# Optimization experiments

Hardware: AMD Instinct MI355X
Metric: run time of the kernel (lower is better)

## Reference

```python
import jax, jax.numpy as jnp
import numpy as np
import math

N, IN, OUT, E, K = 50000, 256, 256, 800000, 32

def setup_inputs() -> dict:
    key = jax.random.key(0)
    k0, k1, k2, k3, k4 = jax.random.split(key, 5)
    feat = jax.random.normal(k0, (N, IN), dtype=jnp.float32)
    # xavier_uniform with relu gain, as in reset_parameters
    gain = math.sqrt(2.0)
    a = gain * math.sqrt(6.0 / (IN + OUT))
    W_self = jax.random.uniform(k1, (OUT, IN), minval=-a, maxval=a, dtype=jnp.float32)
    W_neigh = jax.random.uniform(k2, (OUT, IN), minval=-a, maxval=a, dtype=jnp.float32)
    b_neigh = jnp.zeros((OUT,), dtype=jnp.float32)
    # random CSR graph: E edges, row pointers from sorted cut points
    indices = jax.random.randint(k3, (E,), 0, N, dtype=jnp.int32)
    inner = jnp.sort(jax.random.randint(k4, (N - 1,), 0, E, dtype=jnp.int32))
    indptr = jnp.concatenate([jnp.zeros((1,), jnp.int32), inner,
                              jnp.full((1,), E, jnp.int32)])
    return {"feat": feat, "W_self": W_self, "W_neigh": W_neigh,
            "b_neigh": b_neigh, "indices": indices, "indptr": indptr}

def reference(feat, W_self, W_neigh, b_neigh, indices, indptr):
    n = feat.shape[0]
    # feat_drop with p=0.0 is identity
    h_self = feat @ W_self.T                      # [N, OUT]
    feat_neigh = feat @ W_neigh.T + b_neigh       # [N, OUT]
    # MaxK: keep top-k entries per row, zero the rest
    vals, idx = jax.lax.top_k(feat_neigh, K)      # [N, K]
    rows = jnp.arange(n)[:, None]
    masked = jnp.zeros_like(feat_neigh).at[rows, idx].set(vals)
    # CSR SpMM with unit values (sum over neighbors)
    deg = indptr[1:] - indptr[:-1]                # [N]
    dst = jnp.repeat(jnp.arange(n, dtype=jnp.int32), deg,
                     total_repeat_length=indices.shape[0])
    h_neigh = jax.ops.segment_sum(masked[indices], dst, num_segments=n)
    return h_self + h_neigh
```

## Files before the change

### kernel.cpp

```cpp
#include <hip/hip_runtime.h>

#define N_NODES 50000
#define TOPK 32
#define SOFT_DELTA 2e-5f

typedef unsigned long long u64;
typedef unsigned u32;
typedef float f32x16 __attribute__((ext_vector_type(16)));
typedef __bf16 bf16x8 __attribute__((ext_vector_type(8)));

__device__ __forceinline__ float dec(u32 u) {
    return __builtin_bit_cast(float, (u & 0x80000000u) ? (u & 0x7FFFFFFFu) : ~u);
}
__device__ __forceinline__ int mbcnt64(u64 m) {
    return __builtin_amdgcn_mbcnt_hi((u32)(m >> 32),
           __builtin_amdgcn_mbcnt_lo((u32)m, 0u));
}

__device__ __forceinline__ u32 enc4(float v, int col) {
    return ((u32)col << 16) |
           ((__builtin_bit_cast(u32, v) + 0x8000u) >> 16);
}

__device__ __forceinline__ u32 s2(float x0, float x1, float& r0, float& r1) {
    const u32 h0 = (__builtin_bit_cast(u32, x0) + 0x8000u) & 0xFFFF0000u;
    const u32 h1 = (__builtin_bit_cast(u32, x1) + 0x8000u) & 0xFFFF0000u;
    r0 = x0 - __builtin_bit_cast(float, h0);
    r1 = x1 - __builtin_bit_cast(float, h1);
    return (h0 >> 16) | h1;
}
__device__ __forceinline__ u32 p2(float x0, float x1) {
    return (((__builtin_bit_cast(u32, x0) + 0x8000u) & 0xFFFF0000u) >> 16) |
           ((__builtin_bit_cast(u32, x1) + 0x8000u) & 0xFFFF0000u);
}

struct Tri { uint4 h1, h2, h3; };
__device__ __forceinline__ Tri cvt8(const float4 u, const float4 v, bool deep) {
    Tri t;
    float r0,r1,r2,r3,r4,r5,r6,r7;
    t.h1.x = s2(u.x, u.y, r0, r1);
    t.h1.y = s2(u.z, u.w, r2, r3);
    t.h1.z = s2(v.x, v.y, r4, r5);
    t.h1.w = s2(v.z, v.w, r6, r7);
    float s0,s1,s2_,s3,s4,s5,s6,s7;
    t.h2.x = s2(r0, r1, s0, s1);
    t.h2.y = s2(r2, r3, s2_, s3);
    t.h2.z = s2(r4, r5, s4, s5);
    t.h2.w = s2(r6, r7, s6, s7);
    if (deep) {
        t.h3.x = p2(s0, s1); t.h3.y = p2(s2_, s3);
        t.h3.z = p2(s4, s5); t.h3.w = p2(s6, s7);
    } else {
        t.h3 = make_uint4(0, 0, 0, 0);
    }
    return t;
}

__global__ __launch_bounds__(256, 2) void gemm_kernel(
    const float* __restrict__ feat,
    const float* __restrict__ Wself,
    const float* __restrict__ Wneigh,
    const float* __restrict__ bneigh,
    float* __restrict__ hself,
    float* __restrict__ fneigh)
{
    __shared__ uint4 LA1[512], LA2[512], LA3[512];
    __shared__ uint4 LB1[512], LB2[512], LB3[512];

    const int tid  = threadIdx.x;
    const int lane = tid & 63;
    const int wave = tid >> 6;
    const int wm   = wave >> 1;
    const int wn   = wave & 1;
    const int kg   = lane >> 5;

    const int rowTile = blockIdx.x >> 2;
    const int colTile = blockIdx.x & 3;
    const int row0 = rowTile * 128;
    const float* __restrict__ Wbase = (colTile < 2) ? Wself : Wneigh;
    const int jbase = (colTile & 1) << 7;
    const bool deep = (colTile >= 2);

    const int srow  = tid >> 1;
    const int shalf = tid & 1;
    int gra = row0 + srow;
    if (gra >= N_NODES) gra = 0;
    const float* pa = feat  + (size_t)gra * 256 + shalf * 16;
    const float* pb = Wbase + (size_t)(jbase + srow) * 256 + shalf * 16;
    const int i0 = ((shalf * 2) << 7) + srow;
    const int i1 = i0 + 128;

    const int rA0 = wm * 64 + (lane & 31);
    const int rB0 = wn * 64 + (lane & 31);

    f32x16 acc[2][2];
#pragma unroll
    for (int i = 0; i < 2; ++i)
#pragma unroll
        for (int j = 0; j < 2; ++j) acc[i][j] = (f32x16)0.f;

    float4 va0, va1, va2, va3, vb0, vb1, vb2, vb3;
    va0 = *(const float4*)(pa);      va1 = *(const float4*)(pa + 4);
    va2 = *(const float4*)(pa + 8);  va3 = *(const float4*)(pa + 12);
    vb0 = *(const float4*)(pb);      vb1 = *(const float4*)(pb + 4);
    vb2 = *(const float4*)(pb + 8);  vb3 = *(const float4*)(pb + 12);

    for (int s = 0; s < 8; ++s) {
        __syncthreads();
        {
            const Tri tA0 = cvt8(va0, va1, deep);
            const Tri tA1 = cvt8(va2, va3, deep);
            const Tri tB0 = cvt8(vb0, vb1, deep);
            const Tri tB1 = cvt8(vb2, vb3, deep);
            LA1[i0] = tA0.h1; LA2[i0] = tA0.h2;
            LA1[i1] = tA1.h1; LA2[i1] = tA1.h2;
            LB1[i0] = tB0.h1; LB2[i0] = tB0.h2;
            LB1[i1] = tB1.h1; LB2[i1] = tB1.h2;
            if (deep) {
                LA3[i0] = tA0.h3; LA3[i1] = tA1.h3;
                LB3[i0] = tB0.h3; LB3[i1] = tB1.h3;
            }
        }
        __syncthreads();

        if (s < 7) {
            const int ko = (s + 1) * 32;
            va0 = *(const float4*)(pa + ko);      va1 = *(const float4*)(pa + ko + 4);
            va2 = *(const float4*)(pa + ko + 8);  va3 = *(const float4*)(pa + ko + 12);
            vb0 = *(const float4*)(pb + ko);      vb1 = *(const float4*)(pb + ko + 4);
            vb2 = *(const float4*)(pb + ko + 8);  vb3 = *(const float4*)(pb + ko + 12);
        }

        if (deep) {
#pragma unroll
            for (int ks = 0; ks < 2; ++ks) {
                const int base = ((ks << 1) | kg) << 7;
                bf16x8 a1[2], a2[2], a3[2], b1[2], b2[2], b3[2];
#pragma unroll
                for (int f = 0; f < 2; ++f) {
                    const int ia = base + rA0 + f * 32;
                    const int ib = base + rB0 + f * 32;
                    a1[f] = __builtin_bit_cast(bf16x8, LA1[ia]);
                    a2[f] = __builtin_bit_cast(bf16x8, LA2[ia]);
                    a3[f] = __builtin_bit_cast(bf16x8, LA3[ia]);
                    b1[f] = __builtin_bit_cast(bf16x8, LB1[ib]);
                    b2[f] = __builtin_bit_cast(bf16x8, LB2[ib]);
                    b3[f] = __builtin_bit_cast(bf16x8, LB3[ib]);
                }
#pragma unroll
                for (int i = 0; i < 2; ++i)
#pragma unroll
                    for (int j = 0; j < 2; ++j) {
                        acc[i][j] = __builtin_amdgcn_mfma_f32_32x32x16_bf16(
                            a1[i], b1[j], acc[i][j], 0, 0, 0);
                        acc[i][j] = __builtin_amdgcn_mfma_f32_32x32x16_bf16(
                            a1[i], b2[j], acc[i][j], 0, 0, 0);
                        acc[i][j] = __builtin_amdgcn_mfma_f32_32x32x16_bf16(
                            a2[i], b1[j], acc[i][j], 0, 0, 0);
                        acc[i][j] = __builtin_amdgcn_mfma_f32_32x32x16_bf16(
                            a2[i], b2[j], acc[i][j], 0, 0, 0);
                        acc[i][j] = __builtin_amdgcn_mfma_f32_32x32x16_bf16(
                            a1[i], b3[j], acc[i][j], 0, 0, 0);
                        acc[i][j] = __builtin_amdgcn_mfma_f32_32x32x16_bf16(
                            a3[i], b1[j], acc[i][j], 0, 0, 0);
                    }
            }
        } else {
#pragma unroll
            for (int ks = 0; ks < 2; ++ks) {
                const int base = ((ks << 1) | kg) << 7;
                bf16x8 a1[2], a2[2], b1[2], b2[2];
#pragma unroll
                for (int f = 0; f < 2; ++f) {
                    const int ia = base + rA0 + f * 32;
                    const int ib = base + rB0 + f * 32;
                    a1[f] = __builtin_bit_cast(bf16x8, LA1[ia]);
                    a2[f] = __builtin_bit_cast(bf16x8, LA2[ia]);
                    b1[f] = __builtin_bit_cast(bf16x8, LB1[ib]);
                    b2[f] = __builtin_bit_cast(bf16x8, LB2[ib]);
                }
#pragma unroll
                for (int i = 0; i < 2; ++i)
#pragma unroll
                    for (int j = 0; j < 2; ++j) {
                        acc[i][j] = __builtin_amdgcn_mfma_f32_32x32x16_bf16(
                            a1[i], b1[j], acc[i][j], 0, 0, 0);
                        acc[i][j] = __builtin_amdgcn_mfma_f32_32x32x16_bf16(
                            a1[i], b2[j], acc[i][j], 0, 0, 0);
                        acc[i][j] = __builtin_amdgcn_mfma_f32_32x32x16_bf16(
                            a2[i], b1[j], acc[i][j], 0, 0, 0);
                    }
            }
        }
    }

#pragma unroll
    for (int i = 0; i < 2; ++i) {
        const int rbase = row0 + wm * 64 + i * 32 + (kg << 2);
#pragma unroll
        for (int j = 0; j < 2; ++j) {
            const int cg = (colTile << 7) + wn * 64 + j * 32 + (lane & 31);
            float* dst; int c; float badd;
            if (colTile < 2) { dst = hself;  c = cg;       badd = 0.f; }
            else             { dst = fneigh; c = cg - 256; badd = bneigh[cg - 256]; }
#pragma unroll
            for (int r = 0; r < 16; ++r) {
                const int grow = rbase + (r & 3) + ((r >> 2) << 3);
                if (grow < N_NODES)
                    dst[(size_t)grow * 256 + c] = acc[i][j][r] + badd;
            }
        }
    }
}

__global__ __launch_bounds__(256) void topk_kernel(
    const float* __restrict__ fneigh,
    u32*  __restrict__ compact,
    u64*  __restrict__ softList)
{
    const int lane = threadIdx.x & 63;
    const int wave = threadIdx.x >> 6;
    const int row  = blockIdx.x * 4 + wave;

    const float4 v4 = ((const float4*)(fneigh + (size_t)row * 256))[lane];
    const float vv[4] = {v4.x, v4.y, v4.z, v4.w};
    u32 key[4];
#pragma unroll
    for (int j = 0; j < 4; ++j) {
        const u32 b = __builtin_bit_cast(u32, vv[j]);
        key[j] = (b & 0x80000000u) ? ~b : (b | 0x80000000u);
    }

    u32 T = 0;
    for (int b = 31; b >= 0; --b) {
        const u32 t2 = T | (1u << b);
        int cnt = 0;
#pragma unroll
        for (int j = 0; j < 4; ++j) cnt += __popcll(__ballot(key[j] >= t2));
        if (cnt >= TOPK) T = t2;
    }

    u64 bgt[4], beq[4];
    int cgt = 0, ceq = 0;
#pragma unroll
    for (int j = 0; j < 4; ++j) {
        bgt[j] = __ballot(key[j] > T);
        beq[j] = __ballot(key[j] == T);
        cgt += __popcll(bgt[j]);
        ceq += __popcll(beq[j]);
    }
    const int r = TOPK - cgt;

    u32 m33;
    if (ceq > r) {
        m33 = T;
    } else {
        u32 x = 0;
#pragma unroll
        for (int j = 0; j < 4; ++j) x = max(x, (key[j] < T) ? key[j] : 0u);
#pragma unroll
        for (int off = 32; off >= 1; off >>= 1) x = max(x, (u32)__shfl_xor((int)x, off, 64));
        m33 = x;
    }
    const float v32f = dec(T);
    const float v33f = dec(m33);
    const bool soft = (v32f - v33f) < SOFT_DELTA;

    const int meqsum = mbcnt64(beq[0]) + mbcnt64(beq[1]) +
                       mbcnt64(beq[2]) + mbcnt64(beq[3]);

    int gtbase = 0, selfpre = 0, spillcol = -1;
#pragma unroll
    for (int j = 0; j < 4; ++j) {
        const int col = lane * 4 + j;
        if (key[j] > T) {
            const int pos = gtbase + mbcnt64(bgt[j]);
            compact[(size_t)row * 32 + pos] = enc4(vv[j], col);
        } else if (key[j] == T) {
            const int eqrank = meqsum + selfpre;
            if (eqrank < r) {
                const float w = (soft && eqrank == r - 1) ? 0.5f : 1.0f;
                compact[(size_t)row * 32 + (cgt + eqrank)] = enc4(vv[j] * w, col);
            } else if (eqrank == r) {
                spillcol = col;
            }
            ++selfpre;
        }
        gtbase += __popcll(bgt[j]);
    }

    if (soft) {
        const u64 valbits = (u64)__builtin_bit_cast(u32, 0.5f * v33f);
        if (ceq > r) {
            if (spillcol >= 0)
                softList[row] = (((u64)(u32)spillcol) << 32) | valbits;
        } else {
            int best = 1 << 30;
#pragma unroll
            for (int j = 0; j < 4; ++j) {
                const u64 b33 = __ballot(key[j] == m33);
                if (b33) best = min(best, ((int)__builtin_ctzll(b33)) * 4 + j);
            }
            if (lane == 0)
                softList[row] = (((u64)(u32)best) << 32) | valbits;
        }
    } else if (lane == 0) {
        softList[row] = 0ull;
    }
}

__global__ __launch_bounds__(512) void spmm_kernel(
    const u32* __restrict__ compact,
    const u64* __restrict__ softList,
    const int* __restrict__ indices,
    const int* __restrict__ indptr,
    float* __restrict__ inout)
{
    __shared__ float accs[8][2][256];

    const int lane = threadIdx.x & 63;
    const int wave = threadIdx.x >> 6;
    const int node = blockIdx.x * 8 + wave;
    const int half = lane >> 5;
    const int e    = lane & 31;
    float* acc  = accs[wave][half];

    const float4 z4 = make_float4(0.f, 0.f, 0.f, 0.f);
    ((float4*)&accs[wave][0][0])[lane] = z4;
    ((float4*)&accs[wave][1][0])[lane] = z4;

    const int start = indptr[node];
    const int deg   = indptr[node + 1] - start;
    const float4 hs = ((const float4*)(inout + (size_t)node * 256))[lane];

    for (int base = 0; base < deg; base += 64) {
        const int n = min(64, deg - base);
        const int myidx = (base + lane < deg) ? indices[start + base + lane] : 0;
        for (int d = 0; d < n; d += 16) {
            int s[8]; bool ok[8]; u32 ent[8];
#pragma unroll
            for (int k = 0; k < 8; ++k) {
                const int ei = d + 2 * k + half;
                ok[k] = ei < n;
                s[k]  = __shfl(myidx, min(ei, n - 1), 64);
                ent[k] = compact[(size_t)s[k] * 32 + e];
            }
            u64 se[8];
            if (e == 0) {
#pragma unroll
                for (int k = 0; k < 8; ++k) se[k] = softList[s[k]];
            }
#pragma unroll
            for (int k = 0; k < 8; ++k) {
                const int c = (int)(ent[k] >> 16);
                float v = __builtin_bit_cast(float, ent[k] << 16);
                if (!ok[k]) v = 0.f;
                acc[c] += v;
                if (e == 0 && ok[k]) {
                    const u32 vb = (u32)se[k];
                    if (vb)
                        acc[(int)(se[k] >> 32)] += __builtin_bit_cast(float, vb);
                }
            }
        }
    }

    const float4 a0 = ((const float4*)&accs[wave][0][0])[lane];
    const float4 a1 = ((const float4*)&accs[wave][1][0])[lane];
    float4 o;
    o.x = a0.x + a1.x + hs.x;
    o.y = a0.y + a1.y + hs.y;
    o.z = a0.z + a1.z + hs.z;
    o.w = a0.w + a1.w + hs.w;
    ((float4*)(inout + (size_t)node * 256))[lane] = o;
}

extern "C" void kernel_launch(void* const* d_in, const int* in_sizes, int n_in,
                              void* d_out, int out_size, void* d_ws, size_t ws_size,
                              hipStream_t stream) {
    const float* feat   = (const float*)d_in[0];
    const float* Wself  = (const float*)d_in[1];
    const float* Wneigh = (const float*)d_in[2];
    const float* bneigh = (const float*)d_in[3];
    const int* indices  = (const int*)d_in[4];
    const int* indptr   = (const int*)d_in[5];
    float* out = (float*)d_out;

    char* ws       = (char*)d_ws;
    float* fneigh  = (float*)ws;
    u32*  compact  = (u32*)(ws + (size_t)N_NODES * 256 * 4);
    u64*  softList = (u64*)(ws + (size_t)N_NODES * 256 * 4
                               + (size_t)N_NODES * 32 * 4);

    const int rowTiles = (N_NODES + 127) / 128;
    gemm_kernel<<<dim3(rowTiles * 4), dim3(256), 0, stream>>>(
        feat, Wself, Wneigh, bneigh, out, fneigh);

    const int rowBlocks = N_NODES / 4;
    topk_kernel<<<dim3(rowBlocks), dim3(256), 0, stream>>>(fneigh, compact, softList);

    const int spmmBlocks = N_NODES / 8;
    spmm_kernel<<<dim3(spmmBlocks), dim3(512), 0, stream>>>(
        compact, softList, indices, indptr, out);
}
```

Before: 300.9 us.

## Pre-split weights into bf16 tiles once, stream them directly into LDS

```diff
diff --git a/kernel.cpp b/kernel.cpp
--- a/kernel.cpp
+++ b/kernel.cpp
@@ -56,10 +56,32 @@
     return t;
 }
 
-__global__ __launch_bounds__(256, 2) void gemm_kernel(
+__global__ __launch_bounds__(256) void wprep_kernel(
+    const float* __restrict__ Wself, const float* __restrict__ Wneigh,
+    uint4* __restrict__ WT1, uint4* __restrict__ WT2, uint4* __restrict__ WT3)
+{
+    const int ct = blockIdx.x;
+    const float* __restrict__ Wbase = (ct < 2) ? Wself : Wneigh;
+    const int jbase = (ct & 1) << 7;
+    for (int it = 0; it < 16; ++it) {
+        const int id = it * 256 + threadIdx.x;
+        const int r  = id & 127;
+        const int cc = id >> 7;
+        const int ks = cc >> 2, c = cc & 3;
+        const float* src = Wbase + (size_t)(jbase + r) * 256 + cc * 8;
+        const float4 f0 = *(const float4*)(src);
+        const float4 f1 = *(const float4*)(src + 4);
+        const Tri t = cvt8(f0, f1, true);
+        const int o = ((ct * 8 + ks) * 4 + c) * 128 + r;
+        WT1[o] = t.h1; WT2[o] = t.h2; WT3[o] = t.h3;
+    }
+}
+
+__global__ __launch_bounds__(256, 3) void gemm_kernel(
     const float* __restrict__ feat,
-    const float* __restrict__ Wself,
-    const float* __restrict__ Wneigh,
+    const uint4* __restrict__ WT1,
+    const uint4* __restrict__ WT2,
+    const uint4* __restrict__ WT3,
     const float* __restrict__ bneigh,
     float* __restrict__ hself,
     float* __restrict__ fneigh)
@@ -77,16 +99,13 @@
     const int rowTile = blockIdx.x >> 2;
     const int colTile = blockIdx.x & 3;
     const int row0 = rowTile * 128;
-    const float* __restrict__ Wbase = (colTile < 2) ? Wself : Wneigh;
-    const int jbase = (colTile & 1) << 7;
     const bool deep = (colTile >= 2);
 
     const int srow  = tid >> 1;
     const int shalf = tid & 1;
     int gra = row0 + srow;
     if (gra >= N_NODES) gra = 0;
-    const float* pa = feat  + (size_t)gra * 256 + shalf * 16;
-    const float* pb = Wbase + (size_t)(jbase + srow) * 256 + shalf * 16;
+    const float* pa = feat + (size_t)gra * 256 + shalf * 16;
     const int i0 = ((shalf * 2) << 7) + srow;
     const int i1 = i0 + 128;
 
@@ -99,27 +118,30 @@
 #pragma unroll
         for (int j = 0; j < 2; ++j) acc[i][j] = (f32x16)0.f;
 
-    float4 va0, va1, va2, va3, vb0, vb1, vb2, vb3;
+    float4 va0, va1, va2, va3;
     va0 = *(const float4*)(pa);      va1 = *(const float4*)(pa + 4);
     va2 = *(const float4*)(pa + 8);  va3 = *(const float4*)(pa + 12);
-    vb0 = *(const float4*)(pb);      vb1 = *(const float4*)(pb + 4);
-    vb2 = *(const float4*)(pb + 8);  vb3 = *(const float4*)(pb + 12);
+
+    uint4 ub0, ub1, ub2, ub3;
+    uint4 ub4 = make_uint4(0,0,0,0), ub5 = make_uint4(0,0,0,0);
+    {
+        const int wb = (colTile * 8 + 0) * 512;
+        ub0 = WT1[wb + tid]; ub1 = WT1[wb + tid + 256];
+        ub2 = WT2[wb + tid]; ub3 = WT2[wb + tid + 256];
+        if (deep) { ub4 = WT3[wb + tid]; ub5 = WT3[wb + tid + 256]; }
+    }
 
     for (int s = 0; s < 8; ++s) {
         __syncthreads();
         {
             const Tri tA0 = cvt8(va0, va1, deep);
             const Tri tA1 = cvt8(va2, va3, deep);
-            const Tri tB0 = cvt8(vb0, vb1, deep);
-            const Tri tB1 = cvt8(vb2, vb3, deep);
             LA1[i0] = tA0.h1; LA2[i0] = tA0.h2;
             LA1[i1] = tA1.h1; LA2[i1] = tA1.h2;
-            LB1[i0] = tB0.h1; LB2[i0] = tB0.h2;
-            LB1[i1] = tB1.h1; LB2[i1] = tB1.h2;
-            if (deep) {
-                LA3[i0] = tA0.h3; LA3[i1] = tA1.h3;
-                LB3[i0] = tB0.h3; LB3[i1] = tB1.h3;
-            }
+            if (deep) { LA3[i0] = tA0.h3; LA3[i1] = tA1.h3; }
+            LB1[tid] = ub0; LB1[tid + 256] = ub1;
+            LB2[tid] = ub2; LB2[tid + 256] = ub3;
+            if (deep) { LB3[tid] = ub4; LB3[tid + 256] = ub5; }
         }
         __syncthreads();
 
@@ -127,8 +149,10 @@
             const int ko = (s + 1) * 32;
             va0 = *(const float4*)(pa + ko);      va1 = *(const float4*)(pa + ko + 4);
             va2 = *(const float4*)(pa + ko + 8);  va3 = *(const float4*)(pa + ko + 12);
-            vb0 = *(const float4*)(pb + ko);      vb1 = *(const float4*)(pb + ko + 4);
-            vb2 = *(const float4*)(pb + ko + 8);  vb3 = *(const float4*)(pb + ko + 12);
+            const int wb = (colTile * 8 + s + 1) * 512;
+            ub0 = WT1[wb + tid]; ub1 = WT1[wb + tid + 256];
+            ub2 = WT2[wb + tid]; ub3 = WT2[wb + tid + 256];
+            if (deep) { ub4 = WT3[wb + tid]; ub5 = WT3[wb + tid + 256]; }
         }
 
         if (deep) {
@@ -391,10 +415,18 @@
     u32*  compact  = (u32*)(ws + (size_t)N_NODES * 256 * 4);
     u64*  softList = (u64*)(ws + (size_t)N_NODES * 256 * 4
                                + (size_t)N_NODES * 32 * 4);
+    char* wtbase   = ws + (size_t)N_NODES * 256 * 4
+                        + (size_t)N_NODES * 32 * 4
+                        + (size_t)N_NODES * 8;
+    uint4* WT1 = (uint4*)(wtbase);
+    uint4* WT2 = (uint4*)(wtbase + 4 * 65536);
+    uint4* WT3 = (uint4*)(wtbase + 8 * 65536);
+
+    wprep_kernel<<<dim3(4), dim3(256), 0, stream>>>(Wself, Wneigh, WT1, WT2, WT3);
 
     const int rowTiles = (N_NODES + 127) / 128;
     gemm_kernel<<<dim3(rowTiles * 4), dim3(256), 0, stream>>>(
-        feat, Wself, Wneigh, bneigh, out, fneigh);
+        feat, WT1, WT2, WT3, bneigh, out, fneigh);
 
     const int rowBlocks = N_NODES / 4;
     topk_kernel<<<dim3(rowBlocks), dim3(256), 0, stream>>>(fneigh, compact, softList);
```

New measurement: 436.4 us. 45.1% more time.
